# Optimization experiments

Measured on AMD Instinct MI355X. Metric: run time of the kernel, lower is better.

The kernel has to match this reference:

```python
import jax, jax.numpy as jnp
import numpy as np

N_NODES = 50000
N_EDGES = 1_600_000
D_IN = 128
D_HID = 128
N_CLASSES = 8
N_GRAPHS = 64


def setup_inputs() -> dict:
    key = jax.random.key(0)
    ks = jax.random.split(key, 8)
    x = jax.random.normal(ks[0], (N_NODES, D_IN), dtype=jnp.float32)
    edge_index = jax.random.randint(ks[1], (2, N_EDGES), 0, N_NODES, dtype=jnp.int32)
    graph_ids = jnp.sort(jax.random.randint(ks[2], (N_NODES,), 0, N_GRAPHS, dtype=jnp.int32))
    s = 1.0 / np.sqrt(D_HID)
    W1 = jax.random.normal(ks[3], (D_IN, D_HID), dtype=jnp.float32) * s
    b1 = jnp.zeros((D_HID,), dtype=jnp.float32)
    W2 = jax.random.normal(ks[4], (D_HID, D_HID), dtype=jnp.float32) * s
    b2 = jnp.zeros((D_HID,), dtype=jnp.float32)
    Wc = jax.random.normal(ks[5], (D_HID, N_CLASSES), dtype=jnp.float32) * s
    bc = jnp.zeros((N_CLASSES,), dtype=jnp.float32)
    return {"x": x, "edge_index": edge_index, "graph_ids": graph_ids,
            "W1": W1, "b1": b1, "W2": W2, "b2": b2, "Wc": Wc, "bc": bc}


def _gcn_layer(h, src, dst, norm, W, b):
    # message: gather source features, apply symmetric degree normalization
    msg = h[src] * norm[:, None]                       # [E, d]
    agg = jax.ops.segment_sum(msg, dst, num_segments=N_NODES)  # [N, d]
    return jax.nn.relu(agg @ W + b)


def reference(x, edge_index, graph_ids, W1, b1, W2, b2, Wc, bc):
    src, dst = edge_index[0], edge_index[1]
    ones_e = jnp.ones((N_EDGES,), dtype=x.dtype)
    deg = jax.ops.segment_sum(ones_e, dst, num_segments=N_NODES)
    deg_inv_sqrt = jnp.where(deg > 0, jax.lax.rsqrt(jnp.maximum(deg, 1.0)), 0.0)
    norm = deg_inv_sqrt[src] * deg_inv_sqrt[dst]       # [E]

    h = _gcn_layer(x, src, dst, norm, W1, b1)
    h = _gcn_layer(h, src, dst, norm, W2, b2)

    # per-graph mean pooling (segment mean over nodes of each graph)
    ones_n = jnp.ones((N_NODES,), dtype=h.dtype)
    counts = jax.ops.segment_sum(ones_n, graph_ids, num_segments=N_GRAPHS)
    pooled = jax.ops.segment_sum(h, graph_ids, num_segments=N_GRAPHS)
    pooled = pooled / jnp.maximum(counts, 1.0)[:, None]  # [G, d]

    logits = pooled @ Wc + bc                           # [G, n_classes]
    return logits
```

## Files before the change

kernel.cpp:

```cpp
#include <hip/hip_runtime.h>
#include <hip/hip_bf16.h>

#define D_HID 128
#define N_GRAPHS 64
#define N_CLASSES 8
#define NPB 16
#define CAP 96
#define KSWEEP 4

__device__ inline unsigned short f2b(float x) {
    unsigned int u = __float_as_uint(x);
    unsigned int r = (u + 0x7fffu + ((u >> 16) & 1u)) >> 16;
    return (unsigned short)r;
}
__device__ inline float b2f(unsigned short u) {
    return __uint_as_float((unsigned int)u << 16);
}

__global__ __launch_bounds__(256) void prep_kernel(const float* __restrict__ x,
                                                   uint2* __restrict__ xb4,
                                                   int castBlocks, int n4,
                                                   const int* __restrict__ src,
                                                   const int* __restrict__ dst,
                                                   int* __restrict__ cursor,
                                                   unsigned short* __restrict__ csr16,
                                                   int E, int N, int fillBlocks, int rangeSize) {
    const int b = blockIdx.x;
    if (b < castBlocks) {
        int i = b * 256 + threadIdx.x;
        if (i < n4) {
            float4 v = ((const float4*)x)[i];
            uint2 o;
            o.x = (unsigned int)f2b(v.x) | ((unsigned int)f2b(v.y) << 16);
            o.y = (unsigned int)f2b(v.z) | ((unsigned int)f2b(v.w) << 16);
            xb4[i] = o;
        }
        return;
    }
    const int fb = b - castBlocks;
    const int sweep = fb / fillBlocks;
    const int blk = fb - sweep * fillBlocks;
    const int e = blk * 256 + threadIdx.x;
    if (e >= E) return;
    const int s = src[e];
    const int lo = sweep * rangeSize;
    if (s < lo || s >= lo + rangeSize) return;
    const int d = dst[e];
    int slot = atomicAdd(&cursor[d], 1);
    if (slot < CAP) csr16[(size_t)slot * N + d] = (unsigned short)s;
}

__global__ __launch_bounds__(256) void layer_kernel(const unsigned short* __restrict__ h_in,
                                                    const int* __restrict__ deg,
                                                    const unsigned short* __restrict__ csr16,
                                                    const float* __restrict__ W,
                                                    const float* __restrict__ bias,
                                                    unsigned short* __restrict__ h_out,
                                                    int N) {
    const int base = blockIdx.x * NPB;
    const int tid = threadIdx.x;
    const int wv = tid >> 6;
    const int lane = tid & 63;
    const int q = lane >> 4;
    const int ql = lane & 15;
    __shared__ float s_agg[NPB][D_HID];

    const int n0 = base + wv * 4;
    float acc[4][8] = {};
    int dd[4];
    float dnv[4];
    #pragma unroll
    for (int i = 0; i < 4; ++i) {
        const int n = n0 + i;
        const int dg = (n < N) ? deg[n] : 0;
        dd[i] = min(dg, CAP);
        dnv[i] = (dg > 0) ? rsqrtf((float)dg) : 0.0f;
    }
    const int dm = max(max(dd[0], dd[1]), max(dd[2], dd[3]));

    for (int cb = 0; cb < dm; cb += 64) {
        const int cm = min(64, dm - cb);
        unsigned int pk[4];
        #pragma unroll
        for (int i = 0; i < 4; ++i) {
            pk[i] = 0u;
            if (lane < dd[i] - cb) {
                unsigned int u = (unsigned int)csr16[(size_t)(cb + lane) * N + (n0 + i)];
                const int du = deg[u];
                const float wu = (du > 0) ? rsqrtf((float)du) : 0.0f;
                pk[i] = u | ((unsigned int)f2b(wu) << 16);
            }
        }
        #pragma unroll 4
        for (int j = 0; j < cm; j += 4) {
            const int e = j + q;
            #pragma unroll
            for (int i = 0; i < 4; ++i) {
                const unsigned int p = (unsigned int)__shfl((int)pk[i], e);
                const float w = __uint_as_float(p & 0xffff0000u);
                const uint4 r = *(const uint4*)&h_in[(size_t)(p & 0xffffu) * D_HID + ql * 8];
                acc[i][0] = fmaf(w, __uint_as_float(r.x << 16), acc[i][0]);
                acc[i][1] = fmaf(w, __uint_as_float(r.x & 0xffff0000u), acc[i][1]);
                acc[i][2] = fmaf(w, __uint_as_float(r.y << 16), acc[i][2]);
                acc[i][3] = fmaf(w, __uint_as_float(r.y & 0xffff0000u), acc[i][3]);
                acc[i][4] = fmaf(w, __uint_as_float(r.z << 16), acc[i][4]);
                acc[i][5] = fmaf(w, __uint_as_float(r.z & 0xffff0000u), acc[i][5]);
                acc[i][6] = fmaf(w, __uint_as_float(r.w << 16), acc[i][6]);
                acc[i][7] = fmaf(w, __uint_as_float(r.w & 0xffff0000u), acc[i][7]);
            }
        }
    }

    #pragma unroll
    for (int i = 0; i < 4; ++i) {
        #pragma unroll
        for (int k = 0; k < 8; ++k) {
            acc[i][k] += __shfl_down(acc[i][k], 32);
            acc[i][k] += __shfl_down(acc[i][k], 16);
        }
        if (q == 0) {
            #pragma unroll
            for (int k = 0; k < 8; ++k) s_agg[wv * 4 + i][ql * 8 + k] = acc[i][k] * dnv[i];
        }
    }
    __syncthreads();

    const int t = tid & 127;
    const int nb = tid >> 7;
    float outv[8];
    const float bt = bias[t];
    #pragma unroll
    for (int i = 0; i < 8; ++i) outv[i] = bt;

    for (int k = 0; k < D_HID; k += 4) {
        const float w0 = W[(k + 0) * D_HID + t];
        const float w1 = W[(k + 1) * D_HID + t];
        const float w2 = W[(k + 2) * D_HID + t];
        const float w3 = W[(k + 3) * D_HID + t];
        #pragma unroll
        for (int i = 0; i < 8; ++i) {
            float4 a = *(const float4*)&s_agg[nb * 8 + i][k];
            outv[i] = fmaf(a.x, w0, outv[i]);
            outv[i] = fmaf(a.y, w1, outv[i]);
            outv[i] = fmaf(a.z, w2, outv[i]);
            outv[i] = fmaf(a.w, w3, outv[i]);
        }
    }

    #pragma unroll
    for (int i = 0; i < 8; ++i) {
        const int n = base + nb * 8 + i;
        if (n >= N) break;
        h_out[(size_t)n * D_HID + t] = f2b(fmaxf(outv[i], 0.0f));
    }
}

__global__ __launch_bounds__(128) void pool_classify_kernel(const unsigned short* __restrict__ h,
                                                            const int* __restrict__ gid,
                                                            const float* __restrict__ Wc,
                                                            const float* __restrict__ bc,
                                                            float* __restrict__ out, int N) {
    const int g = blockIdx.x;
    const int t = threadIdx.x;
    int lo = 0, hi = N;
    while (lo < hi) { int mid = (lo + hi) >> 1; if (gid[mid] < g) lo = mid + 1; else hi = mid; }
    int lo1 = lo, hi1 = N;
    while (lo1 < hi1) { int mid = (lo1 + hi1) >> 1; if (gid[mid] < g + 1) lo1 = mid + 1; else hi1 = mid; }
    const int cnt = lo1 - lo;

    float sum = 0.0f;
    int n = lo;
    for (; n + 4 <= lo1; n += 4) {
        float a0 = b2f(h[(size_t)(n + 0) * D_HID + t]);
        float a1 = b2f(h[(size_t)(n + 1) * D_HID + t]);
        float a2 = b2f(h[(size_t)(n + 2) * D_HID + t]);
        float a3 = b2f(h[(size_t)(n + 3) * D_HID + t]);
        sum += (a0 + a1) + (a2 + a3);
    }
    for (; n < lo1; ++n) sum += b2f(h[(size_t)n * D_HID + t]);

    __shared__ float sp[D_HID];
    sp[t] = sum;
    __syncthreads();

    if (t < N_CLASSES) {
        const float inv = 1.0f / fmaxf((float)cnt, 1.0f);
        float acc = bc[t];
        #pragma unroll 8
        for (int k = 0; k < D_HID; ++k) {
            acc = fmaf(sp[k] * inv, Wc[k * N_CLASSES + t], acc);
        }
        out[g * N_CLASSES + t] = acc;
    }
}

extern "C" void kernel_launch(void* const* d_in, const int* in_sizes, int n_in,
                              void* d_out, int out_size, void* d_ws, size_t ws_size,
                              hipStream_t stream) {
    const float* x   = (const float*)d_in[0];
    const int* edge  = (const int*)d_in[1];
    const int* gid   = (const int*)d_in[2];
    const float* W1  = (const float*)d_in[3];
    const float* b1  = (const float*)d_in[4];
    const float* W2  = (const float*)d_in[5];
    const float* b2  = (const float*)d_in[6];
    const float* Wc  = (const float*)d_in[7];
    const float* bc  = (const float*)d_in[8];
    float* out       = (float*)d_out;

    const int E = in_sizes[1] / 2;
    const int N = in_sizes[2];
    const int* src = edge;
    const int* dst = edge + E;

    char* p = (char*)d_ws;
    auto take = [&](size_t bytes) {
        char* r = p;
        p += (bytes + 255) & ~(size_t)255;
        return r;
    };
    int*   cursor  = (int*)take((size_t)N * 4);
    unsigned short* csr16 = (unsigned short*)take((size_t)N * CAP * 2);
    unsigned short* xb  = (unsigned short*)take((size_t)N * D_HID * 2);
    unsigned short* h1b = (unsigned short*)take((size_t)N * D_HID * 2);
    unsigned short* h2b = (unsigned short*)take((size_t)N * D_HID * 2);

    hipMemsetAsync(cursor, 0, (size_t)N * 4, stream);

    const int EB = 256;
    const int n4 = (N * D_HID) / 4;
    const int castBlocks = (n4 + EB - 1) / EB;
    const int fillBlocks = (E + EB - 1) / EB;
    const int rangeSize = (N + KSWEEP - 1) / KSWEEP;
    prep_kernel<<<castBlocks + KSWEEP * fillBlocks, EB, 0, stream>>>(
        x, (uint2*)xb, castBlocks, n4, src, dst, cursor, csr16, E, N, fillBlocks, rangeSize);

    const int LG = (N + NPB - 1) / NPB;
    layer_kernel<<<LG, 256, 0, stream>>>(xb, cursor, csr16, W1, b1, h1b, N);
    layer_kernel<<<LG, 256, 0, stream>>>(h1b, cursor, csr16, W2, b2, h2b, N);

    pool_classify_kernel<<<N_GRAPHS, 128, 0, stream>>>(h2b, gid, Wc, bc, out, N);
}
```

Before: 389.3 us.

## Split pooling across many blocks with atomics and add separate classify kernel

The old pooling kernel used only 64 blocks, one per graph, and each block walked about 780 nodes serially. The new pool_kernel assigns 8 contiguous nodes to each of roughly 6250 blocks. Each block keeps a running sum while the graph id stays the same and flushes it to a zeroed fp32 pooled buffer with atomicAdd. A single-block classify kernel then does the mean division and the matmul against Wc. The change adds a memset, one extra launch and atomic contention on 64x128 floats, and the float sum order is no longer fixed.

Result: faster. 346.1 us (-11.1%).

```diff
diff --git a/kernel.cpp b/kernel.cpp
--- a/kernel.cpp
+++ b/kernel.cpp
@@ -155,43 +155,45 @@
     }
 }
 
-__global__ __launch_bounds__(128) void pool_classify_kernel(const unsigned short* __restrict__ h,
-                                                            const int* __restrict__ gid,
-                                                            const float* __restrict__ Wc,
-                                                            const float* __restrict__ bc,
-                                                            float* __restrict__ out, int N) {
-    const int g = blockIdx.x;
+__global__ __launch_bounds__(128) void pool_kernel(const unsigned short* __restrict__ h,
+                                                   const int* __restrict__ gid,
+                                                   float* __restrict__ pooled,
+                                                   int N, int nodes_per_block) {
     const int t = threadIdx.x;
+    const int start = blockIdx.x * nodes_per_block;
+    if (start >= N) return;
+    const int endn = min(start + nodes_per_block, N);
+    int cur = gid[start];
+    float sum = 0.0f;
+    for (int n = start; n < endn; ++n) {
+        int g = gid[n];
+        if (g != cur) {
+            atomicAdd(&pooled[cur * D_HID + t], sum);
+            cur = g; sum = 0.0f;
+        }
+        sum += b2f(h[(size_t)n * D_HID + t]);
+    }
+    atomicAdd(&pooled[cur * D_HID + t], sum);
+}
+
+__global__ __launch_bounds__(512) void classify_kernel(const float* __restrict__ pooled,
+                                                       const int* __restrict__ gid,
+                                                       const float* __restrict__ Wc,
+                                                       const float* __restrict__ bc,
+                                                       float* __restrict__ out, int N) {
+    const int g = threadIdx.x >> 3;
+    const int c = threadIdx.x & 7;
     int lo = 0, hi = N;
     while (lo < hi) { int mid = (lo + hi) >> 1; if (gid[mid] < g) lo = mid + 1; else hi = mid; }
     int lo1 = lo, hi1 = N;
     while (lo1 < hi1) { int mid = (lo1 + hi1) >> 1; if (gid[mid] < g + 1) lo1 = mid + 1; else hi1 = mid; }
-    const int cnt = lo1 - lo;
-
-    float sum = 0.0f;
-    int n = lo;
-    for (; n + 4 <= lo1; n += 4) {
-        float a0 = b2f(h[(size_t)(n + 0) * D_HID + t]);
-        float a1 = b2f(h[(size_t)(n + 1) * D_HID + t]);
-        float a2 = b2f(h[(size_t)(n + 2) * D_HID + t]);
-        float a3 = b2f(h[(size_t)(n + 3) * D_HID + t]);
-        sum += (a0 + a1) + (a2 + a3);
-    }
-    for (; n < lo1; ++n) sum += b2f(h[(size_t)n * D_HID + t]);
-
-    __shared__ float sp[D_HID];
-    sp[t] = sum;
-    __syncthreads();
-
-    if (t < N_CLASSES) {
-        const float inv = 1.0f / fmaxf((float)cnt, 1.0f);
-        float acc = bc[t];
-        #pragma unroll 8
-        for (int k = 0; k < D_HID; ++k) {
-            acc = fmaf(sp[k] * inv, Wc[k * N_CLASSES + t], acc);
-        }
-        out[g * N_CLASSES + t] = acc;
-    }
+    const float inv = 1.0f / fmaxf((float)(lo1 - lo), 1.0f);
+    float acc = bc[c];
+    #pragma unroll 8
+    for (int k = 0; k < D_HID; ++k) {
+        acc = fmaf(pooled[g * D_HID + k] * inv, Wc[k * N_CLASSES + c], acc);
+    }
+    out[g * N_CLASSES + c] = acc;
 }
 
 extern "C" void kernel_launch(void* const* d_in, const int* in_sizes, int n_in,
@@ -220,12 +222,14 @@
         return r;
     };
     int*   cursor  = (int*)take((size_t)N * 4);
+    float* pooled  = (float*)take((size_t)N_GRAPHS * D_HID * 4);
     unsigned short* csr16 = (unsigned short*)take((size_t)N * CAP * 2);
     unsigned short* xb  = (unsigned short*)take((size_t)N * D_HID * 2);
     unsigned short* h1b = (unsigned short*)take((size_t)N * D_HID * 2);
     unsigned short* h2b = (unsigned short*)take((size_t)N * D_HID * 2);
 
     hipMemsetAsync(cursor, 0, (size_t)N * 4, stream);
+    hipMemsetAsync(pooled, 0, (size_t)N_GRAPHS * D_HID * 4, stream);
 
     const int EB = 256;
     const int n4 = (N * D_HID) / 4;
@@ -239,5 +243,7 @@
     layer_kernel<<<LG, 256, 0, stream>>>(xb, cursor, csr16, W1, b1, h1b, N);
     layer_kernel<<<LG, 256, 0, stream>>>(h1b, cursor, csr16, W2, b2, h2b, N);
 
-    pool_classify_kernel<<<N_GRAPHS, 128, 0, stream>>>(h2b, gid, Wc, bc, out, N);
-}
+    const int NPBLK = 8;
+    pool_kernel<<<(N + NPBLK - 1) / NPBLK, 128, 0, stream>>>(h2b, gid, pooled, N, NPBLK);
+    classify_kernel<<<1, 512, 0, stream>>>(pooled, gid, Wc, bc, out, N);
+}
```
